# Performance work log

Measured on AMD Instinct MI355X. Metric: run time of the kernel, lower is better.

The kernel has to match this reference:

```python
import jax, jax.numpy as jnp
import numpy as np

DIM = 2048
INTER = 1408
N_EXPERTS = 16
TOP_K = 2
N_SHARED = 2
SHARED_INTER = N_SHARED * INTER  # 2816


def setup_inputs() -> dict:
    key = jax.random.key(0)
    ks = jax.random.split(key, 9)
    s = 0.02
    return {
        "x": jax.random.normal(ks[0], (4, 2048, DIM), dtype=jnp.float32),
        "gate_w": jax.random.normal(ks[1], (N_EXPERTS, DIM), dtype=jnp.float32) * s,
        "w1": jax.random.normal(ks[2], (N_EXPERTS, INTER, DIM), dtype=jnp.float32) * s,
        "w2": jax.random.normal(ks[3], (N_EXPERTS, DIM, INTER), dtype=jnp.float32) * s,
        "w3": jax.random.normal(ks[4], (N_EXPERTS, INTER, DIM), dtype=jnp.float32) * s,
        "sw1": jax.random.normal(ks[5], (SHARED_INTER, DIM), dtype=jnp.float32) * s,
        "sw2": jax.random.normal(ks[6], (DIM, SHARED_INTER), dtype=jnp.float32) * s,
        "sw3": jax.random.normal(ks[7], (SHARED_INTER, DIM), dtype=jnp.float32) * s,
    }


def _swiglu(t, wa, wb, wo):
    # t: [T, d_in]; wa, wb: [d_h, d_in]; wo: [d_out, d_h]
    h = jax.nn.silu(t @ wa.T) * (t @ wb.T)
    return h @ wo.T


def reference(x, gate_w, w1, w2, w3, sw1, sw2, sw3):
    shape = x.shape
    t = x.reshape(-1, DIM)                      # [T, dim]
    scores = jax.nn.softmax(t @ gate_w.T, axis=-1)  # [T, E]
    weights, indices = jax.lax.top_k(scores, TOP_K)  # [T, k] each

    y = jnp.zeros_like(t)
    # Small fixed loop over experts (structurally distinct weights).
    # Per-token combine weight for expert e: sum over top-k slots routed to e
    # (matches y[idx] += expert(x[idx]) * weights[idx, top]; zero weight for
    # unrouted tokens reproduces the counts[i]==0 skip exactly).
    for e in range(N_EXPERTS):
        w_e = jnp.sum(jnp.where(indices == e, weights, 0.0), axis=-1)  # [T]
        y = y + _swiglu(t, w1[e], w3[e], w2[e]) * w_e[:, None]

    z = _swiglu(t, sw1, sw3, sw2)               # shared experts MLP
    return (y + z).reshape(shape)
```

## Files before the change

### kernel.cpp

```cpp
#include <hip/hip_runtime.h>
#include <hip/hip_bf16.h>

#define DIM 2048
#define INTER 1408
#define NEXP 16
#define NTOK 8192
#define SINTER 2816

typedef __attribute__((ext_vector_type(8))) short bf16x8;
typedef __attribute__((ext_vector_type(4))) float f32x4;
typedef __attribute__((ext_vector_type(8))) unsigned short u16x8;

__device__ __forceinline__ unsigned short f2bf(float f) {
    union { float f; unsigned u; } a; a.f = f;
    unsigned r = a.u + 0x7fffu + ((a.u >> 16) & 1u);
    return (unsigned short)(r >> 16);
}

__device__ __forceinline__ void gload16(const void* g, void* lds) {
    __builtin_amdgcn_global_load_lds(
        (const __attribute__((address_space(1))) void*)g,
        (__attribute__((address_space(3))) void*)lds, 16, 0, 0);
}

__global__ __launch_bounds__(256) void cast_bf16(const float* __restrict__ s,
                                                 unsigned short* __restrict__ d,
                                                 long long n) {
    long long i = ((long long)blockIdx.x * 256 + threadIdx.x) * 8;
    if (i >= n) return;
    float4 a = *(const float4*)(s + i), b = *(const float4*)(s + i + 4);
    u16x8 o = { f2bf(a.x), f2bf(a.y), f2bf(a.z), f2bf(a.w),
                f2bf(b.x), f2bf(b.y), f2bf(b.z), f2bf(b.w) };
    *(u16x8*)(d + i) = o;
}

__global__ __launch_bounds__(256) void gate_topk(
    const float* __restrict__ x, const float* __restrict__ gw,
    int* __restrict__ counts, int* __restrict__ toklist, float* __restrict__ tokw) {
    int wave = threadIdx.x >> 6;
    int lane = threadIdx.x & 63;
    int tok  = blockIdx.x * 4 + wave;
    const float* xr = x + (size_t)tok * DIM;

    float part[NEXP];
#pragma unroll
    for (int e = 0; e < NEXP; ++e) part[e] = 0.f;
#pragma unroll
    for (int c = 0; c < DIM / 256; ++c) {
        float4 xv = *(const float4*)(xr + c * 256 + lane * 4);
#pragma unroll
        for (int e = 0; e < NEXP; ++e) {
            float4 g = *(const float4*)(gw + e * DIM + c * 256 + lane * 4);
            part[e] += xv.x * g.x + xv.y * g.y + xv.z * g.z + xv.w * g.w;
        }
    }
#pragma unroll
    for (int e = 0; e < NEXP; ++e) {
        float v = part[e];
#pragma unroll
        for (int off = 32; off; off >>= 1) v += __shfl_xor(v, off);
        part[e] = v;
    }
    float mx = part[0];
#pragma unroll
    for (int e = 1; e < NEXP; ++e) mx = fmaxf(mx, part[e]);
    float Z = 0.f;
#pragma unroll
    for (int e = 0; e < NEXP; ++e) Z += expf(part[e] - mx);
    int i1 = 0; float m1 = part[0];
#pragma unroll
    for (int e = 1; e < NEXP; ++e) if (part[e] > m1) { m1 = part[e]; i1 = e; }
    int i2 = -1; float m2 = -1e30f;
#pragma unroll
    for (int e = 0; e < NEXP; ++e) if (e != i1 && part[e] > m2) { m2 = part[e]; i2 = e; }
    if (lane == 0) {
        float w1v = expf(m1 - mx) / Z;
        float w2v = expf(m2 - mx) / Z;
        int p1 = atomicAdd(&counts[i1], 1);
        toklist[i1 * NTOK + p1] = tok; tokw[i1 * NTOK + p1] = w1v;
        int p2 = atomicAdd(&counts[i2], 1);
        toklist[i2 * NTOK + p2] = tok; tokw[i2 * NTOK + p2] = w2v;
    }
}

__global__ void prefix_k(const int* __restrict__ counts, int* __restrict__ base) {
    if (threadIdx.x == 0) {
        int acc = 0;
        for (int e = 0; e < NEXP; ++e) { base[e] = acc; acc += counts[e]; }
        base[16] = acc;
        base[17] = acc + NTOK;
    }
}

__device__ __forceinline__ int swz(int r) { return (r ^ (r >> 2)) & 3; }

__global__ __launch_bounds__(512, 2) void gemm1(
    const unsigned short* __restrict__ xb,
    const unsigned short* __restrict__ w1b, const unsigned short* __restrict__ w3b,
    const unsigned short* __restrict__ sw1b, const unsigned short* __restrict__ sw3b,
    const int* __restrict__ counts, const int* __restrict__ base,
    const int* __restrict__ toklist, unsigned short* __restrict__ hbuf) {
    const int e   = blockIdx.z;
    const int cnt = (e < NEXP) ? counts[e] : NTOK;
    const int m0  = blockIdx.y * 256;
    if (m0 >= cnt) return;
    const int n0  = blockIdx.x * 128;
    const size_t woff = (size_t)((e < NEXP) ? e : e - NEXP) * INTER * DIM;
    const unsigned short* B1 = ((e < NEXP) ? w1b : sw1b) + woff;
    const unsigned short* B3 = ((e < NEXP) ? w3b : sw3b) + woff;
    const int hbase = base[e];
    const int* tl = toklist + e * NTOK;

    __shared__ __attribute__((aligned(16))) unsigned short As[4][8192];
    __shared__ __attribute__((aligned(16))) unsigned short B1s[4][4096];
    __shared__ __attribute__((aligned(16))) unsigned short B3s[4][4096];

    const int tid = threadIdx.x;
    const int w = tid >> 6, l = tid & 63;
    const int wr = w >> 1, wc = w & 1;
    const int lr = l & 15, hi = l >> 4;

    const int row0 = tid >> 2, row1 = row0 + 128;
    const int c0 = (tid & 3) ^ swz(row0);
    int g0 = m0 + row0, g1 = m0 + row1;
    int t0, t1;
    if (e < NEXP) { t0 = (g0 < cnt) ? tl[g0] : 0; t1 = (g1 < cnt) ? tl[g1] : 0; }
    else          { t0 = g0; t1 = g1; }
    const unsigned short* aSrc0 = xb + (size_t)t0 * DIM + c0 * 8;
    const unsigned short* aSrc1 = xb + (size_t)t1 * DIM + c0 * 8;
    const unsigned short* b1Src = B1 + (size_t)(n0 + row0) * DIM + c0 * 8;
    const unsigned short* b3Src = B3 + (size_t)(n0 + row0) * DIM + c0 * 8;

    int aoff[4], boff[4];
#pragma unroll
    for (int m = 0; m < 4; ++m) {
        int r = wr * 64 + m * 16 + lr;
        aoff[m] = r * 64 + ((swz(r) ^ hi) << 4);
    }
#pragma unroll
    for (int n = 0; n < 4; ++n) {
        int r = wc * 64 + n * 16 + lr;
        boff[n] = r * 64 + ((swz(r) ^ hi) << 4);
    }

    f32x4 acc1[4][4], acc3[4][4];
#pragma unroll
    for (int m = 0; m < 4; ++m)
#pragma unroll
        for (int n = 0; n < 4; ++n) {
            acc1[m][n] = (f32x4){0.f, 0.f, 0.f, 0.f};
            acc3[m][n] = (f32x4){0.f, 0.f, 0.f, 0.f};
        }

    const int H = DIM / 32;

    auto STAGE = [&](int hh) {
        int hb = hh & 3;
        int kc = hh * 32;
        gload16(aSrc0 + kc, &As[hb][tid * 8]);
        gload16(aSrc1 + kc, &As[hb][4096 + tid * 8]);
        gload16(b1Src + kc, &B1s[hb][tid * 8]);
        gload16(b3Src + kc, &B3s[hb][tid * 8]);
    };

    STAGE(0); STAGE(1); STAGE(2);
    asm volatile("s_waitcnt vmcnt(8)" ::: "memory");
    __builtin_amdgcn_s_barrier();

    for (int h = 0; h < H; ++h) {
        const int hb = h & 3;
        bf16x8 af[4], b1f[4], b3f[4];
#pragma unroll
        for (int m = 0; m < 4; ++m)
            af[m] = *(const bf16x8*)((const char*)&As[hb][0] + aoff[m]);
#pragma unroll
        for (int n = 0; n < 4; ++n) {
            b1f[n] = *(const bf16x8*)((const char*)&B1s[hb][0] + boff[n]);
            b3f[n] = *(const bf16x8*)((const char*)&B3s[hb][0] + boff[n]);
        }
        if (h + 3 < H) {
            STAGE(h + 3);
            asm volatile("s_waitcnt vmcnt(8)" ::: "memory");
        } else if (h == H - 3) {
            asm volatile("s_waitcnt vmcnt(4)" ::: "memory");
        } else if (h == H - 2) {
            asm volatile("s_waitcnt vmcnt(0)" ::: "memory");
        }
        __builtin_amdgcn_s_barrier();
        asm volatile("s_waitcnt lgkmcnt(0)" ::: "memory");
        __builtin_amdgcn_sched_barrier(0);
        __builtin_amdgcn_s_setprio(1);
#pragma unroll
        for (int m = 0; m < 4; ++m)
#pragma unroll
            for (int n = 0; n < 4; ++n) {
                acc1[m][n] = __builtin_amdgcn_mfma_f32_16x16x32_bf16(af[m], b1f[n], acc1[m][n], 0, 0, 0);
                acc3[m][n] = __builtin_amdgcn_mfma_f32_16x16x32_bf16(af[m], b3f[n], acc3[m][n], 0, 0, 0);
            }
        __builtin_amdgcn_s_setprio(0);
        __builtin_amdgcn_s_barrier();
    }

#pragma unroll
    for (int m = 0; m < 4; ++m) {
#pragma unroll
        for (int i = 0; i < 4; ++i) {
            int row  = wr * 64 + m * 16 + hi * 4 + i;
            int grow = m0 + row;
            if (grow < cnt) {
                size_t ro = (size_t)(hbase + grow) * INTER;
#pragma unroll
                for (int n = 0; n < 4; ++n) {
                    int col = n0 + wc * 64 + n * 16 + lr;
                    float a = acc1[m][n][i];
                    float hv = a / (1.f + __expf(-a)) * acc3[m][n][i];
                    hbuf[ro + col] = f2bf(hv);
                }
            }
        }
    }
}

__global__ __launch_bounds__(512, 2) void gemm2(
    const unsigned short* __restrict__ hbuf,
    const unsigned short* __restrict__ w2b, const unsigned short* __restrict__ sw2b,
    const int* __restrict__ counts, const int* __restrict__ base,
    const int* __restrict__ toklist, const float* __restrict__ tokw,
    float* __restrict__ out) {
    const int e   = blockIdx.z;
    const int cnt = (e < NEXP) ? counts[e] : NTOK;
    const int m0  = blockIdx.y * 256;
    if (m0 >= cnt) return;
    const int n0  = blockIdx.x * 256;
    const int hbase = base[e];
    const size_t bstride = (e < NEXP) ? INTER : SINTER;
    const unsigned short* Bb = (e < NEXP) ? w2b + (size_t)e * DIM * INTER
                                          : sw2b + (size_t)(e - NEXP) * INTER;

    __shared__ __attribute__((aligned(16))) unsigned short Ah[4][8192];
    __shared__ __attribute__((aligned(16))) unsigned short Bh[4][8192];

    const int tid = threadIdx.x;
    const int w = tid >> 6, l = tid & 63;
    const int wr = w >> 2, wc = w & 3;
    const int lr = l & 15, hi = l >> 4;

    const int row0 = tid >> 2, row1 = row0 + 128;
    const int c0 = (tid & 3) ^ swz(row0);
    const unsigned short* aSrc0 = hbuf + (size_t)(hbase + m0 + row0) * INTER + c0 * 8;
    const unsigned short* aSrc1 = hbuf + (size_t)(hbase + m0 + row1) * INTER + c0 * 8;
    const unsigned short* bSrc0 = Bb + (size_t)(n0 + row0) * bstride + c0 * 8;
    const unsigned short* bSrc1 = Bb + (size_t)(n0 + row1) * bstride + c0 * 8;

    int aoff[8], boff[4];
#pragma unroll
    for (int m = 0; m < 8; ++m) {
        int r = wr * 128 + m * 16 + lr;
        aoff[m] = r * 64 + ((swz(r) ^ hi) << 4);
    }
#pragma unroll
    for (int n = 0; n < 4; ++n) {
        int r = wc * 64 + n * 16 + lr;
        boff[n] = r * 64 + ((swz(r) ^ hi) << 4);
    }

    f32x4 acc[8][4];
#pragma unroll
    for (int m = 0; m < 8; ++m)
#pragma unroll
        for (int n = 0; n < 4; ++n) acc[m][n] = (f32x4){0.f, 0.f, 0.f, 0.f};

    const int H = INTER / 32;

    auto STAGE = [&](int hh) {
        int hb = hh & 3;
        int kc = hh * 32;
        gload16(aSrc0 + kc, &Ah[hb][tid * 8]);
        gload16(aSrc1 + kc, &Ah[hb][4096 + tid * 8]);
        gload16(bSrc0 + kc, &Bh[hb][tid * 8]);
        gload16(bSrc1 + kc, &Bh[hb][4096 + tid * 8]);
    };

    STAGE(0); STAGE(1); STAGE(2);
    asm volatile("s_waitcnt vmcnt(8)" ::: "memory");
    __builtin_amdgcn_s_barrier();

    for (int h = 0; h < H; ++h) {
        const int hb = h & 3;
        bf16x8 af[8], bf[4];
#pragma unroll
        for (int m = 0; m < 8; ++m)
            af[m] = *(const bf16x8*)((const char*)&Ah[hb][0] + aoff[m]);
#pragma unroll
        for (int n = 0; n < 4; ++n)
            bf[n] = *(const bf16x8*)((const char*)&Bh[hb][0] + boff[n]);
        if (h + 3 < H) {
            STAGE(h + 3);
            asm volatile("s_waitcnt vmcnt(8)" ::: "memory");
        } else if (h == H - 3) {
            asm volatile("s_waitcnt vmcnt(4)" ::: "memory");
        } else if (h == H - 2) {
            asm volatile("s_waitcnt vmcnt(0)" ::: "memory");
        }
        __builtin_amdgcn_s_barrier();
        asm volatile("s_waitcnt lgkmcnt(0)" ::: "memory");
        __builtin_amdgcn_sched_barrier(0);
        __builtin_amdgcn_s_setprio(1);
#pragma unroll
        for (int m = 0; m < 8; ++m)
#pragma unroll
            for (int n = 0; n < 4; ++n)
                acc[m][n] = __builtin_amdgcn_mfma_f32_16x16x32_bf16(af[m], bf[n], acc[m][n], 0, 0, 0);
        __builtin_amdgcn_s_setprio(0);
        __builtin_amdgcn_s_barrier();
    }

#pragma unroll
    for (int m = 0; m < 8; ++m) {
#pragma unroll
        for (int i = 0; i < 4; ++i) {
            int row  = wr * 128 + m * 16 + hi * 4 + i;
            int grow = m0 + row;
            if (grow < cnt) {
                int tok; float wt;
                if (e < NEXP) { tok = toklist[e * NTOK + grow]; wt = tokw[e * NTOK + grow]; }
                else          { tok = grow; wt = 1.f; }
                float* orow = out + (size_t)tok * DIM + n0 + wc * 64 + lr;
#pragma unroll
                for (int n = 0; n < 4; ++n)
                    unsafeAtomicAdd(orow + n * 16, acc[m][n][i] * wt);
            }
        }
    }
}

extern "C" void kernel_launch(void* const* d_in, const int* in_sizes, int n_in,
                              void* d_out, int out_size, void* d_ws, size_t ws_size,
                              hipStream_t stream) {
    const float* x   = (const float*)d_in[0];
    const float* gw  = (const float*)d_in[1];
    const float* w1  = (const float*)d_in[2];
    const float* w2  = (const float*)d_in[3];
    const float* w3  = (const float*)d_in[4];
    const float* sw1 = (const float*)d_in[5];
    const float* sw2 = (const float*)d_in[6];
    const float* sw3 = (const float*)d_in[7];
    float* out = (float*)d_out;

    char* ws = (char*)d_ws;
    int*   counts  = (int*)ws;
    int*   basep   = (int*)(ws + 128);
    int*   toklist = (int*)(ws + 4096);
    float* tokw    = (float*)(ws + 4096 + (size_t)NEXP * NTOK * 4);
    unsigned short* hbuf = (unsigned short*)(ws + (2u << 20));

    const size_t hbytes = (size_t)4 * NTOK * INTER * 2;
    const size_t offx   = (2ull << 20) + hbytes;
    const size_t xbytes = (size_t)NTOK * DIM * 2;
    const size_t offw   = offx + xbytes;
    const size_t wB     = (size_t)NEXP * INTER * DIM * 2;
    const size_t swB    = (size_t)SINTER * DIM * 2;

    unsigned short* xb   = (unsigned short*)(ws + offx);
    unsigned short* w1b  = (unsigned short*)(ws + offw);
    unsigned short* w3b  = (unsigned short*)(ws + offw + wB);
    unsigned short* w2b  = (unsigned short*)(ws + offw + 2 * wB);
    unsigned short* sw1b = (unsigned short*)(ws + offw + 3 * wB);
    unsigned short* sw3b = (unsigned short*)(ws + offw + 3 * wB + swB);
    unsigned short* sw2b = (unsigned short*)(ws + offw + 3 * wB + 2 * swB);

    hipMemsetAsync(counts, 0, 64, stream);
    hipMemsetAsync(d_out, 0, (size_t)out_size * sizeof(float), stream);

    gate_topk<<<NTOK / 4, 256, 0, stream>>>(x, gw, counts, toklist, tokw);
    prefix_k<<<1, 64, 0, stream>>>(counts, basep);

    auto cast = [&](const float* s, unsigned short* d, long long n) {
        cast_bf16<<<(int)((n / 8 + 255) / 256), 256, 0, stream>>>(s, d, n);
    };
    cast(x, xb, (long long)NTOK * DIM);
    cast(w1, w1b, (long long)NEXP * INTER * DIM);
    cast(w3, w3b, (long long)NEXP * INTER * DIM);
    cast(w2, w2b, (long long)NEXP * INTER * DIM);
    cast(sw1, sw1b, (long long)SINTER * DIM);
    cast(sw3, sw3b, (long long)SINTER * DIM);
    cast(sw2, sw2b, (long long)SINTER * DIM);

    gemm1<<<dim3(INTER / 128, NTOK / 256, 18), 512, 0, stream>>>(
        xb, w1b, w3b, sw1b, sw3b, counts, basep, toklist, hbuf);
    gemm2<<<dim3(DIM / 256, NTOK / 256, 18), 512, 0, stream>>>(
        hbuf, w2b, sw2b, counts, basep, toklist, tokw, out);
}
```

Baseline: 1.352 ms.

## Double-buffer fragment reads in GEMMs, shrink gemm2 tile, fuse x cast into gating

Both GEMM main loops are restructured to ping-pong two register fragment sets, so LDS reads for step h+1 are issued while the MFMAs for step h run, and one barrier per step is dropped. gemm2's output tile goes from 256x256 to 256x128, which halves the B staging buffer and accumulator registers and doubles the grid. The activation cast to bf16 is folded into the gating kernel, removing one launch and one extra read of x. The costs are more register pressure from the duplicated fragments, more gemm2 blocks each rereading the A tiles, and a tighter hand-tuned waitcnt schedule that has to stay correct.

```diff
diff --git a/kernel.cpp b/kernel.cpp
--- a/kernel.cpp
+++ b/kernel.cpp
@@ -9,7 +9,12 @@
 
 typedef __attribute__((ext_vector_type(8))) short bf16x8;
 typedef __attribute__((ext_vector_type(4))) float f32x4;
+typedef __attribute__((ext_vector_type(4))) unsigned short u16x4;
 typedef __attribute__((ext_vector_type(8))) unsigned short u16x8;
+
+#define VMCNT(n) asm volatile("s_waitcnt vmcnt(" #n ")" ::: "memory")
+#define BARRIER() __builtin_amdgcn_s_barrier()
+#define SCHEDB() __builtin_amdgcn_sched_barrier(0)
 
 __device__ __forceinline__ unsigned short f2bf(float f) {
     union { float f; unsigned u; } a; a.f = f;
@@ -36,11 +41,13 @@
 
 __global__ __launch_bounds__(256) void gate_topk(
     const float* __restrict__ x, const float* __restrict__ gw,
+    unsigned short* __restrict__ xb,
     int* __restrict__ counts, int* __restrict__ toklist, float* __restrict__ tokw) {
     int wave = threadIdx.x >> 6;
     int lane = threadIdx.x & 63;
     int tok  = blockIdx.x * 4 + wave;
     const float* xr = x + (size_t)tok * DIM;
+    unsigned short* xbr = xb + (size_t)tok * DIM;
 
     float part[NEXP];
 #pragma unroll
@@ -48,6 +55,8 @@
 #pragma unroll
     for (int c = 0; c < DIM / 256; ++c) {
         float4 xv = *(const float4*)(xr + c * 256 + lane * 4);
+        u16x4 xo = { f2bf(xv.x), f2bf(xv.y), f2bf(xv.z), f2bf(xv.w) };
+        *(u16x4*)(xbr + c * 256 + lane * 4) = xo;
 #pragma unroll
         for (int e = 0; e < NEXP; ++e) {
             float4 g = *(const float4*)(gw + e * DIM + c * 256 + lane * 4);
@@ -162,43 +171,51 @@
         gload16(b1Src + kc, &B1s[hb][tid * 8]);
         gload16(b3Src + kc, &B3s[hb][tid * 8]);
     };
-
-    STAGE(0); STAGE(1); STAGE(2);
-    asm volatile("s_waitcnt vmcnt(8)" ::: "memory");
-    __builtin_amdgcn_s_barrier();
-
-    for (int h = 0; h < H; ++h) {
-        const int hb = h & 3;
-        bf16x8 af[4], b1f[4], b3f[4];
+    auto READF = [&](bf16x8 (&af)[4], bf16x8 (&b1)[4], bf16x8 (&b3)[4], int hh) {
+        int hb = hh & 3;
+        const char* As_ = (const char*)&As[hb][0];
+        const char* B1_ = (const char*)&B1s[hb][0];
+        const char* B3_ = (const char*)&B3s[hb][0];
+#pragma unroll
+        for (int m = 0; m < 4; ++m) af[m] = *(const bf16x8*)(As_ + aoff[m]);
+#pragma unroll
+        for (int n = 0; n < 4; ++n) {
+            b1[n] = *(const bf16x8*)(B1_ + boff[n]);
+            b3[n] = *(const bf16x8*)(B3_ + boff[n]);
+        }
+    };
+    auto MMA = [&](bf16x8 (&af)[4], bf16x8 (&b1)[4], bf16x8 (&b3)[4]) {
+        __builtin_amdgcn_s_setprio(1);
 #pragma unroll
         for (int m = 0; m < 4; ++m)
-            af[m] = *(const bf16x8*)((const char*)&As[hb][0] + aoff[m]);
-#pragma unroll
-        for (int n = 0; n < 4; ++n) {
-            b1f[n] = *(const bf16x8*)((const char*)&B1s[hb][0] + boff[n]);
-            b3f[n] = *(const bf16x8*)((const char*)&B3s[hb][0] + boff[n]);
-        }
-        if (h + 3 < H) {
-            STAGE(h + 3);
-            asm volatile("s_waitcnt vmcnt(8)" ::: "memory");
-        } else if (h == H - 3) {
-            asm volatile("s_waitcnt vmcnt(4)" ::: "memory");
-        } else if (h == H - 2) {
-            asm volatile("s_waitcnt vmcnt(0)" ::: "memory");
-        }
-        __builtin_amdgcn_s_barrier();
-        asm volatile("s_waitcnt lgkmcnt(0)" ::: "memory");
-        __builtin_amdgcn_sched_barrier(0);
-        __builtin_amdgcn_s_setprio(1);
-#pragma unroll
-        for (int m = 0; m < 4; ++m)
 #pragma unroll
             for (int n = 0; n < 4; ++n) {
-                acc1[m][n] = __builtin_amdgcn_mfma_f32_16x16x32_bf16(af[m], b1f[n], acc1[m][n], 0, 0, 0);
-                acc3[m][n] = __builtin_amdgcn_mfma_f32_16x16x32_bf16(af[m], b3f[n], acc3[m][n], 0, 0, 0);
+                acc1[m][n] = __builtin_amdgcn_mfma_f32_16x16x32_bf16(af[m], b1[n], acc1[m][n], 0, 0, 0);
+                acc3[m][n] = __builtin_amdgcn_mfma_f32_16x16x32_bf16(af[m], b3[n], acc3[m][n], 0, 0, 0);
             }
         __builtin_amdgcn_s_setprio(0);
-        __builtin_amdgcn_s_barrier();
+    };
+
+    bf16x8 afA[4], b1A[4], b3A[4], afB[4], b1B[4], b3B[4];
+
+    STAGE(0); STAGE(1); STAGE(2);
+    VMCNT(8);
+    BARRIER();
+    READF(afA, b1A, b3A, 0);
+
+    for (int h = 0; h < H; h += 2) {
+        if (h + 3 < H) { STAGE(h + 3); VMCNT(8); }
+        else if (h == H - 2) { VMCNT(0); }
+        BARRIER();
+        READF(afB, b1B, b3B, h + 1);
+        SCHEDB();
+        MMA(afA, b1A, b3A);
+        if (h + 4 < H) { STAGE(h + 4); VMCNT(8); }
+        else if (h + 1 == H - 3) { VMCNT(4); }
+        BARRIER();
+        READF(afA, b1A, b3A, h + 2);
+        SCHEDB();
+        MMA(afB, b1B, b3B);
     }
 
 #pragma unroll
@@ -231,31 +248,30 @@
     const int cnt = (e < NEXP) ? counts[e] : NTOK;
     const int m0  = blockIdx.y * 256;
     if (m0 >= cnt) return;
-    const int n0  = blockIdx.x * 256;
+    const int n0  = blockIdx.x * 128;
     const int hbase = base[e];
     const size_t bstride = (e < NEXP) ? INTER : SINTER;
     const unsigned short* Bb = (e < NEXP) ? w2b + (size_t)e * DIM * INTER
                                           : sw2b + (size_t)(e - NEXP) * INTER;
 
     __shared__ __attribute__((aligned(16))) unsigned short Ah[4][8192];
-    __shared__ __attribute__((aligned(16))) unsigned short Bh[4][8192];
+    __shared__ __attribute__((aligned(16))) unsigned short Bh[4][4096];
 
     const int tid = threadIdx.x;
     const int w = tid >> 6, l = tid & 63;
-    const int wr = w >> 2, wc = w & 3;
+    const int wr = w >> 1, wc = w & 1;
     const int lr = l & 15, hi = l >> 4;
 
     const int row0 = tid >> 2, row1 = row0 + 128;
     const int c0 = (tid & 3) ^ swz(row0);
     const unsigned short* aSrc0 = hbuf + (size_t)(hbase + m0 + row0) * INTER + c0 * 8;
     const unsigned short* aSrc1 = hbuf + (size_t)(hbase + m0 + row1) * INTER + c0 * 8;
-    const unsigned short* bSrc0 = Bb + (size_t)(n0 + row0) * bstride + c0 * 8;
-    const unsigned short* bSrc1 = Bb + (size_t)(n0 + row1) * bstride + c0 * 8;
-
-    int aoff[8], boff[4];
-#pragma unroll
-    for (int m = 0; m < 8; ++m) {
-        int r = wr * 128 + m * 16 + lr;
+    const unsigned short* bSrc  = Bb + (size_t)(n0 + row0) * bstride + c0 * 8;
+
+    int aoff[4], boff[4];
+#pragma unroll
+    for (int m = 0; m < 4; ++m) {
+        int r = wr * 64 + m * 16 + lr;
         aoff[m] = r * 64 + ((swz(r) ^ hi) << 4);
     }
 #pragma unroll
@@ -264,9 +280,9 @@
         boff[n] = r * 64 + ((swz(r) ^ hi) << 4);
     }
 
-    f32x4 acc[8][4];
-#pragma unroll
-    for (int m = 0; m < 8; ++m)
+    f32x4 acc[4][4];
+#pragma unroll
+    for (int m = 0; m < 4; ++m)
 #pragma unroll
         for (int n = 0; n < 4; ++n) acc[m][n] = (f32x4){0.f, 0.f, 0.f, 0.f};
 
@@ -277,49 +293,54 @@
         int kc = hh * 32;
         gload16(aSrc0 + kc, &Ah[hb][tid * 8]);
         gload16(aSrc1 + kc, &Ah[hb][4096 + tid * 8]);
-        gload16(bSrc0 + kc, &Bh[hb][tid * 8]);
-        gload16(bSrc1 + kc, &Bh[hb][4096 + tid * 8]);
-    };
-
-    STAGE(0); STAGE(1); STAGE(2);
-    asm volatile("s_waitcnt vmcnt(8)" ::: "memory");
-    __builtin_amdgcn_s_barrier();
-
-    for (int h = 0; h < H; ++h) {
-        const int hb = h & 3;
-        bf16x8 af[8], bf[4];
-#pragma unroll
-        for (int m = 0; m < 8; ++m)
-            af[m] = *(const bf16x8*)((const char*)&Ah[hb][0] + aoff[m]);
-#pragma unroll
-        for (int n = 0; n < 4; ++n)
-            bf[n] = *(const bf16x8*)((const char*)&Bh[hb][0] + boff[n]);
-        if (h + 3 < H) {
-            STAGE(h + 3);
-            asm volatile("s_waitcnt vmcnt(8)" ::: "memory");
-        } else if (h == H - 3) {
-            asm volatile("s_waitcnt vmcnt(4)" ::: "memory");
-        } else if (h == H - 2) {
-            asm volatile("s_waitcnt vmcnt(0)" ::: "memory");
-        }
-        __builtin_amdgcn_s_barrier();
-        asm volatile("s_waitcnt lgkmcnt(0)" ::: "memory");
-        __builtin_amdgcn_sched_barrier(0);
+        gload16(bSrc  + kc, &Bh[hb][tid * 8]);
+    };
+    auto READF = [&](bf16x8 (&af)[4], bf16x8 (&bf)[4], int hh) {
+        int hb = hh & 3;
+        const char* A_ = (const char*)&Ah[hb][0];
+        const char* B_ = (const char*)&Bh[hb][0];
+#pragma unroll
+        for (int m = 0; m < 4; ++m) af[m] = *(const bf16x8*)(A_ + aoff[m]);
+#pragma unroll
+        for (int n = 0; n < 4; ++n) bf[n] = *(const bf16x8*)(B_ + boff[n]);
+    };
+    auto MMA = [&](bf16x8 (&af)[4], bf16x8 (&bf)[4]) {
         __builtin_amdgcn_s_setprio(1);
 #pragma unroll
-        for (int m = 0; m < 8; ++m)
+        for (int m = 0; m < 4; ++m)
 #pragma unroll
             for (int n = 0; n < 4; ++n)
                 acc[m][n] = __builtin_amdgcn_mfma_f32_16x16x32_bf16(af[m], bf[n], acc[m][n], 0, 0, 0);
         __builtin_amdgcn_s_setprio(0);
-        __builtin_amdgcn_s_barrier();
-    }
-
-#pragma unroll
-    for (int m = 0; m < 8; ++m) {
+    };
+
+    bf16x8 afA[4], bfA[4], afB[4], bfB[4];
+
+    STAGE(0); STAGE(1); STAGE(2);
+    VMCNT(6);
+    BARRIER();
+    READF(afA, bfA, 0);
+
+    for (int h = 0; h < H; h += 2) {
+        if (h + 3 < H) { STAGE(h + 3); VMCNT(6); }
+        else if (h == H - 2) { VMCNT(0); }
+        BARRIER();
+        READF(afB, bfB, h + 1);
+        SCHEDB();
+        MMA(afA, bfA);
+        if (h + 4 < H) { STAGE(h + 4); VMCNT(6); }
+        else if (h + 1 == H - 3) { VMCNT(3); }
+        BARRIER();
+        READF(afA, bfA, h + 2);
+        SCHEDB();
+        MMA(afB, bfB);
+    }
+
+#pragma unroll
+    for (int m = 0; m < 4; ++m) {
 #pragma unroll
         for (int i = 0; i < 4; ++i) {
-            int row  = wr * 128 + m * 16 + hi * 4 + i;
+            int row  = wr * 64 + m * 16 + hi * 4 + i;
             int grow = m0 + row;
             if (grow < cnt) {
                 int tok; float wt;
@@ -372,13 +393,12 @@
     hipMemsetAsync(counts, 0, 64, stream);
     hipMemsetAsync(d_out, 0, (size_t)out_size * sizeof(float), stream);
 
-    gate_topk<<<NTOK / 4, 256, 0, stream>>>(x, gw, counts, toklist, tokw);
+    gate_topk<<<NTOK / 4, 256, 0, stream>>>(x, gw, xb, counts, toklist, tokw);
     prefix_k<<<1, 64, 0, stream>>>(counts, basep);
 
     auto cast = [&](const float* s, unsigned short* d, long long n) {
         cast_bf16<<<(int)((n / 8 + 255) / 256), 256, 0, stream>>>(s, d, n);
     };
-    cast(x, xb, (long long)NTOK * DIM);
     cast(w1, w1b, (long long)NEXP * INTER * DIM);
     cast(w3, w3b, (long long)NEXP * INTER * DIM);
     cast(w2, w2b, (long long)NEXP * INTER * DIM);
@@ -388,6 +408,6 @@
 
     gemm1<<<dim3(INTER / 128, NTOK / 256, 18), 512, 0, stream>>>(
         xb, w1b, w3b, sw1b, sw3b, counts, basep, toklist, hbuf);
-    gemm2<<<dim3(DIM / 256, NTOK / 256, 18), 512, 0, stream>>>(
+    gemm2<<<dim3(DIM / 128, NTOK / 256, 18), 512, 0, stream>>>(
         hbuf, w2b, sw2b, counts, basep, toklist, tokw, out);
 }
```

Result: slower. 1.444 ms (+6.8%).
